# Optimization experiments

Measured on AMD Instinct MI355X. Metric: run time of the kernel, lower is better.

The kernel has to match this reference:

```python
import jax, jax.numpy as jnp
import numpy as np

# Module config (matches init_kwargs)
N_HEADS = 16
HEAD = 64
SEQ = 4096          # single prefill sequence (cu_seqlens_k = [0, SEQ])
BS = 64             # block_size (both q and k blocks)
LOCAL = 8           # local_blocks
VERT = 8            # vert_stride
NB = SEQ // BS      # number of blocks along seq
SLIDE = max(1, VERT // N_HEADS)  # get_head_sliding_step(16, 8, homo_head=False) -> 1
SM_SCALE = 1.0 / float(np.sqrt(HEAD))


def _build_layout():
    """Per-head block-sparse layout: causal + (local OR strided-vertical) blocks,
    padded to a fixed max nnz per row (CSR rows -> padded col indices + valid mask)."""
    h = np.arange(N_HEADS)[:, None, None]
    i = np.arange(NB)[None, :, None]
    j = np.arange(NB)[None, None, :]
    mask = (j <= i) & (((i - j) < LOCAL) | (((j + h * SLIDE + 1) % VERT) == 0))
    max_nnz = int(mask.sum(-1).max())
    cols = np.zeros((N_HEADS, NB, max_nnz), np.int32)
    valid = np.zeros((N_HEADS, NB, max_nnz), bool)
    for hh in range(N_HEADS):
        for ii in range(NB):
            c = np.nonzero(mask[hh, ii])[0]
            cols[hh, ii, :len(c)] = c
            valid[hh, ii, :len(c)] = True
    return cols, valid, max_nnz

_COLS_NP, _VALID_NP, MAX_NNZ = _build_layout()
COLS = jnp.asarray(_COLS_NP)    # [H, NB, NNZ] k-block ids (padded with 0)
VALID = jnp.asarray(_VALID_NP)  # [H, NB, NNZ] padding mask


def setup_inputs() -> dict:
    key = jax.random.key(0)
    kq, kk, kv = jax.random.split(key, 3)
    q = jax.random.normal(kq, (SEQ, N_HEADS, HEAD), jnp.float32)
    k = jax.random.normal(kk, (SEQ, N_HEADS, HEAD), jnp.float32)
    v = jax.random.normal(kv, (SEQ, N_HEADS, HEAD), jnp.float32)
    cu_seqlens_k = jnp.array([0, SEQ], jnp.int32)
    return {"q": q, "k": k, "v": v, "cu_seqlens_k": cu_seqlens_k}


def _attn(q, k, v):
    # [T, H, D] -> [H, NB, BS, D]
    qb = q.transpose(1, 0, 2).reshape(N_HEADS, NB, BS, HEAD)
    kb = k.transpose(1, 0, 2).reshape(N_HEADS, NB, BS, HEAD)
    vb = v.transpose(1, 0, 2).reshape(N_HEADS, NB, BS, HEAD)
    gather = jax.vmap(lambda x, c: x[c])  # per-head block gather
    kg = gather(kb, COLS)  # [H, NB, NNZ, BS, D]
    vg = gather(vb, COLS)  # [H, NB, NNZ, BS, D]
    # block-sparse scores: [H, NB(q blk), BS(m), NNZ(n), BS(j)]
    scores = jnp.einsum('himd,hinjd->himnj', qb, kg) * SM_SCALE
    qpos = jnp.arange(NB)[:, None] * BS + jnp.arange(BS)[None, :]   # [NB, BS]
    kpos = COLS[..., None] * BS + jnp.arange(BS)                    # [H, NB, NNZ, BS]
    allow = VALID[:, :, None, :, None] & (
        qpos[None, :, :, None, None] >= kpos[:, :, None, :, :])
    scores = jnp.where(allow, scores, -jnp.inf)
    p = jax.nn.softmax(scores.reshape(N_HEADS, NB, BS, MAX_NNZ * BS), axis=-1)
    p = p.reshape(N_HEADS, NB, BS, MAX_NNZ, BS)
    out = jnp.einsum('himnj,hinjd->himd', p, vg)
    return out.reshape(N_HEADS, SEQ, HEAD).transpose(1, 0, 2)  # [T, H, D]


def reference(q, k, v, cu_seqlens_k):
    # single-sequence prefill: past_len = 0, q_len == k_len == SEQ
    return _attn(q, k, v)
```

## Files before the change

kernel.cpp:

```cpp
#include <hip/hip_runtime.h>
#include <hip/hip_bf16.h>
#include <math.h>


#define NHEADS 16
#define HDIM   64
#define NBLK   64
#define SEQLEN 4096
#define KP     72
#define NEGBIG (-1.0e30f)

typedef __attribute__((ext_vector_type(8))) short bf16x8;
typedef __attribute__((ext_vector_type(4))) float f32x4;

__device__ __forceinline__ short f2bf(float x) {
    union { float f; unsigned u; } c; c.f = x;
    unsigned u = c.u;
    return (short)((u + 0x7FFFu + ((u >> 16) & 1u)) >> 16);
}
__device__ __forceinline__ short f2bf_trunc(float x) {
    union { float f; unsigned u; } c; c.f = x;
    return (short)(c.u >> 16);
}

__device__ __forceinline__ void load_lds16(const short* g, const short* l) {
    __builtin_amdgcn_global_load_lds(
        (const __attribute__((address_space(1))) void*)g,
        (__attribute__((address_space(3))) void*)l, 16, 0, 0);
}

__device__ __forceinline__ void drain_then_sync() {
    asm volatile("s_waitcnt vmcnt(0)" ::: "memory");
    __syncthreads();
}

__global__ __launch_bounds__(256)
void prep_kernel(const float* __restrict__ k, const float* __restrict__ v,
                 short* __restrict__ kt, short* __restrict__ vt) {
    __shared__ short tile[64 * KP];
    const int b = blockIdx.x;
    const int h = b >> 6, jb = b & 63;
    const int tid = threadIdx.x;

    #pragma unroll
    for (int it = 0; it < 4; ++it) {
        int e = it * 1024 + tid * 4;
        int key = e >> 6, d0 = e & 63;
        float4 f = *(const float4*)(v + ((size_t)(jb * 64 + key) * NHEADS + h) * HDIM + d0);
        tile[(d0 + 0) * KP + key] = f2bf(f.x);
        tile[(d0 + 1) * KP + key] = f2bf(f.y);
        tile[(d0 + 2) * KP + key] = f2bf(f.z);
        tile[(d0 + 3) * KP + key] = f2bf(f.w);
    }
    __syncthreads();
    short* vtile = vt + (size_t)b * 4096;
    #pragma unroll
    for (int ii = 0; ii < 2; ++ii) {
        int idx = ii * 256 + tid;
        int d = idx >> 3, gsw = idx & 7;
        int g = gsw ^ (d & 7);
        bf16x8 val;
        #pragma unroll
        for (int j = 0; j < 8; ++j) {
            int s   = g * 8 + j;
            int key = (s & 32) | (((s >> 2) & 1) << 4) | (((s >> 3) & 3) << 2) | (s & 3);
            val[j]  = tile[d * KP + key];
        }
        *(bf16x8*)(vtile + (size_t)idx * 8) = val;
    }
    short* ktile = kt + (size_t)b * 4096;
    #pragma unroll
    for (int ii = 0; ii < 2; ++ii) {
        int idx = ii * 256 + tid;
        int r = idx >> 3, g = idx & 7;
        const float* src = k + ((size_t)(jb * 64 + r) * NHEADS + h) * HDIM + g * 8;
        float4 f0 = *(const float4*)src;
        float4 f1 = *(const float4*)(src + 4);
        bf16x8 a;
        a[0]=f2bf(f0.x); a[1]=f2bf(f0.y); a[2]=f2bf(f0.z); a[3]=f2bf(f0.w);
        a[4]=f2bf(f1.x); a[5]=f2bf(f1.y); a[6]=f2bf(f1.z); a[7]=f2bf(f1.w);
        int G = r * 8 + (g ^ (r & 7));
        *(bf16x8*)(ktile + (size_t)G * 8) = a;
    }
}

__global__ __launch_bounds__(256, 4)
void attn_kernel(const short* __restrict__ kt, const short* __restrict__ vt,
                 const float* __restrict__ q, float* __restrict__ out) {
    __shared__ __align__(16) short kv[2 * 8192];

    const int b    = blockIdx.x;
    const int h    = ((b & 7) << 1) | ((b >> 3) & 1);
    const int idx  = b >> 4;
    const int qi   = (idx & 1) ? (63 - (idx >> 1)) : (idx >> 1);
    const int tid  = threadIdx.x;
    const int wave = tid >> 6;
    const int ih   = wave >> 1;
    const int jh   = wave & 1;
    const int lane = tid & 63;
    const int l16  = lane & 15;
    const int quad = lane >> 4;

    const int rowbase = qi * 64 + ih * 32;

    const float SC = 0.125f * 1.4426950408889634f;
    bf16x8 a_q[2][2];
    #pragma unroll
    for (int rg = 0; rg < 2; ++rg) {
        const float* qrow = q + ((size_t)(rowbase + rg * 16 + l16) * NHEADS + h) * HDIM;
        #pragma unroll
        for (int kk = 0; kk < 2; ++kk) {
            const float* src = qrow + kk * 32 + quad * 8;
            float4 f0 = *(const float4*)(src);
            float4 f1 = *(const float4*)(src + 4);
            bf16x8 a;
            a[0]=f2bf(f0.x*SC); a[1]=f2bf(f0.y*SC); a[2]=f2bf(f0.z*SC); a[3]=f2bf(f0.w*SC);
            a[4]=f2bf(f1.x*SC); a[5]=f2bf(f1.y*SC); a[6]=f2bf(f1.z*SC); a[7]=f2bf(f1.w*SC);
            a_q[rg][kk] = a;
        }
    }

    bf16x8 ones;
    #pragma unroll
    for (int j = 0; j < 8; ++j) ones[j] = (short)0x3F80;

    f32x4 o[2][4];
    f32x4 lacc[2];
    #pragma unroll
    for (int rg = 0; rg < 2; ++rg) {
        lacc[rg] = (f32x4){0.f,0.f,0.f,0.f};
        #pragma unroll
        for (int ntd = 0; ntd < 4; ++ntd) o[rg][ntd] = (f32x4){0.f,0.f,0.f,0.f};
    }

    const short* kth = kt + (size_t)(h * 64) * 4096;
    const short* vth = vt + (size_t)(h * 64) * 4096;

    const int j0  = (7 - h) & 7;
    const int l0  = (qi > 7) ? (qi - 7) : 0;
    const int nv  = (j0 < l0) ? ((l0 - j0 + 7) >> 3) : 0;
    const int T   = nv + (qi - l0 + 1);

    const int r7   = l16 & 7;
    const int gk0  = (quad ^ r7) * 8;
    const int gk1  = gk0 ^ 32;
    const int gv   = (((jh << 2) | quad) ^ r7) * 8;
    const int rowb = l16 * 64;
    const int krow0 = (jh * 32) * 64;

    {
        const int jb0 = (0 < nv) ? j0 : l0;
        const short* ktb = kth + (size_t)jb0 * 4096;
        const short* vtb = vth + (size_t)jb0 * 4096;
        load_lds16(ktb + (size_t)tid * 8,         &kv[wave * 512]);
        load_lds16(ktb + (size_t)(tid + 256) * 8, &kv[2048 + wave * 512]);
        load_lds16(vtb + (size_t)tid * 8,         &kv[4096 + wave * 512]);
        load_lds16(vtb + (size_t)(tid + 256) * 8, &kv[6144 + wave * 512]);
    }

    for (int t = 0; t < T; ++t) {
        drain_then_sync();

        if (t + 1 < T) {
            const int jn = (t + 1 < nv) ? (j0 + 8 * (t + 1)) : (l0 + (t + 1 - nv));
            const int bo = ((t + 1) & 1) * 8192;
            const short* ktb = kth + (size_t)jn * 4096;
            const short* vtb = vth + (size_t)jn * 4096;
            load_lds16(ktb + (size_t)tid * 8,         &kv[bo + wave * 512]);
            load_lds16(ktb + (size_t)(tid + 256) * 8, &kv[bo + 2048 + wave * 512]);
            load_lds16(vtb + (size_t)tid * 8,         &kv[bo + 4096 + wave * 512]);
            load_lds16(vtb + (size_t)(tid + 256) * 8, &kv[bo + 6144 + wave * 512]);
        }

        const short* kb = &kv[(t & 1) * 8192];
        const short* vb = kb + 4096;
        const bool diag = (t == T - 1);

        __builtin_amdgcn_s_setprio(1);

        bf16x8 kf0[2], kf1[2];
        #pragma unroll
        for (int kg = 0; kg < 2; ++kg) {
            kf0[kg] = *(const bf16x8*)&kb[krow0 + kg * 1024 + rowb + gk0];
            kf1[kg] = *(const bf16x8*)&kb[krow0 + kg * 1024 + rowb + gk1];
        }
        f32x4 s[2][2];
        #pragma unroll
        for (int kg = 0; kg < 2; ++kg) {
            #pragma unroll
            for (int rg = 0; rg < 2; ++rg) {
                f32x4 acc = (f32x4){0.f, 0.f, 0.f, 0.f};
                acc = __builtin_amdgcn_mfma_f32_16x16x32_bf16(kf0[kg], a_q[rg][0], acc, 0, 0, 0);
                acc = __builtin_amdgcn_mfma_f32_16x16x32_bf16(kf1[kg], a_q[rg][1], acc, 0, 0, 0);
                s[kg][rg] = acc;
            }
        }

        bf16x8 vf[4];
        #pragma unroll
        for (int ntd = 0; ntd < 4; ++ntd)
            vf[ntd] = *(const bf16x8*)&vb[ntd * 1024 + rowb + gv];

        short pb[2][2][4];
        #pragma unroll
        for (int kg = 0; kg < 2; ++kg) {
            #pragma unroll
            for (int rg = 0; rg < 2; ++rg) {
                #pragma unroll
                for (int r = 0; r < 4; ++r) {
                    const int keyl = jh * 32 + kg * 16 + quad * 4 + r;
                    const int qrl  = ih * 32 + rg * 16 + l16;
                    float raw = s[kg][rg][r];
                    raw = (diag && (keyl > qrl)) ? NEGBIG : raw;
                    float pv = __builtin_amdgcn_exp2f(raw);
                    pb[kg][rg][r] = f2bf_trunc(pv);
                }
            }
        }

        bf16x8 a_p[2];
        #pragma unroll
        for (int rg = 0; rg < 2; ++rg) {
            bf16x8 a;
            a[0]=pb[0][rg][0]; a[1]=pb[0][rg][1]; a[2]=pb[0][rg][2]; a[3]=pb[0][rg][3];
            a[4]=pb[1][rg][0]; a[5]=pb[1][rg][1]; a[6]=pb[1][rg][2]; a[7]=pb[1][rg][3];
            a_p[rg] = a;
        }

        #pragma unroll
        for (int rg = 0; rg < 2; ++rg) {
            #pragma unroll
            for (int ntd = 0; ntd < 4; ++ntd)
                o[rg][ntd] = __builtin_amdgcn_mfma_f32_16x16x32_bf16(a_p[rg], vf[ntd], o[rg][ntd], 0, 0, 0);
            lacc[rg] = __builtin_amdgcn_mfma_f32_16x16x32_bf16(a_p[rg], ones, lacc[rg], 0, 0, 0);
        }

        __builtin_amdgcn_s_setprio(0);
    }

    __syncthreads();
    f32x4* kvF = (f32x4*)kv;
    if (jh == 1) {
        #pragma unroll
        for (int rg = 0; rg < 2; ++rg) {
            #pragma unroll
            for (int ntd = 0; ntd < 4; ++ntd)
                kvF[(ih * 10 + rg * 4 + ntd) * 64 + lane] = o[rg][ntd];
            kvF[(ih * 10 + 8 + rg) * 64 + lane] = lacc[rg];
        }
    }
    __syncthreads();
    if (jh == 0) {
        #pragma unroll
        for (int rg = 0; rg < 2; ++rg) {
            #pragma unroll
            for (int ntd = 0; ntd < 4; ++ntd)
                o[rg][ntd] += kvF[(ih * 10 + rg * 4 + ntd) * 64 + lane];
            lacc[rg] += kvF[(ih * 10 + 8 + rg) * 64 + lane];
        }
        #pragma unroll
        for (int rg = 0; rg < 2; ++rg) {
            #pragma unroll
            for (int r = 0; r < 4; ++r) {
                const float invr = 1.0f / lacc[rg][r];
                int trow = rowbase + rg * 16 + quad * 4 + r;
                float* orow = out + ((size_t)trow * NHEADS + h) * HDIM;
                #pragma unroll
                for (int ntd = 0; ntd < 4; ++ntd)
                    orow[ntd * 16 + l16] = o[rg][ntd][r] * invr;
            }
        }
    }
}

extern "C" void kernel_launch(void* const* d_in, const int* in_sizes, int n_in,
                              void* d_out, int out_size, void* d_ws, size_t ws_size,
                              hipStream_t stream) {
    const float* q = (const float*)d_in[0];
    const float* k = (const float*)d_in[1];
    const float* v = (const float*)d_in[2];
    float* out = (float*)d_out;

    const size_t tileBytes = (size_t)NHEADS * NBLK * 4096 * sizeof(short);
    short* kt = (short*)d_ws;
    short* vt = (short*)((char*)d_ws + tileBytes);
    prep_kernel<<<dim3(NHEADS * NBLK), dim3(256), 0, stream>>>(k, v, kt, vt);
    attn_kernel<<<dim3(1024), dim3(256), 0, stream>>>(kt, vt, q, out);
}
```

Measured before the change: 111.7 us.

## Split attention block into two independent waves each owning half the keys

Reworks the attention kernel from 4 waves (2 query halves × 2 key halves) to 2 waves, where each wave covers all 64 query rows and loads its own half of each K/V block into private LDS double buffers. This removes the per-iteration block-wide barrier, leaving only a per-wave vmcnt wait, and halves the redundant K/V LDS reads across query halves. The V tile swizzle in the prep kernel is changed to match the new per-wave half-block layout, and the final reduction has each wave finish half of the rows. In exchange each wave holds twice the accumulators (more VGPRs), and with 128-thread blocks there are fewer waves per CU to hide latency.

```diff
diff --git a/kernel.cpp b/kernel.cpp
--- a/kernel.cpp
+++ b/kernel.cpp
@@ -27,11 +27,6 @@
     __builtin_amdgcn_global_load_lds(
         (const __attribute__((address_space(1))) void*)g,
         (__attribute__((address_space(3))) void*)l, 16, 0, 0);
-}
-
-__device__ __forceinline__ void drain_then_sync() {
-    asm volatile("s_waitcnt vmcnt(0)" ::: "memory");
-    __syncthreads();
 }
 
 __global__ __launch_bounds__(256)
@@ -57,8 +52,10 @@
     #pragma unroll
     for (int ii = 0; ii < 2; ++ii) {
         int idx = ii * 256 + tid;
-        int d = idx >> 3, gsw = idx & 7;
-        int g = gsw ^ (d & 7);
+        int jh = idx >> 8;
+        int d  = (idx >> 2) & 63;
+        int qq = idx & 3;
+        int g  = jh * 4 + (qq ^ ((d >> 1) & 3));
         bf16x8 val;
         #pragma unroll
         for (int j = 0; j < 8; ++j) {
@@ -84,30 +81,26 @@
     }
 }
 
-__global__ __launch_bounds__(256, 4)
+__global__ __launch_bounds__(128, 2)
 void attn_kernel(const short* __restrict__ kt, const short* __restrict__ vt,
                  const float* __restrict__ q, float* __restrict__ out) {
-    __shared__ __align__(16) short kv[2 * 8192];
+    __shared__ __align__(16) short kv[16384];
 
     const int b    = blockIdx.x;
     const int h    = ((b & 7) << 1) | ((b >> 3) & 1);
     const int idx  = b >> 4;
     const int qi   = (idx & 1) ? (63 - (idx >> 1)) : (idx >> 1);
     const int tid  = threadIdx.x;
-    const int wave = tid >> 6;
-    const int ih   = wave >> 1;
-    const int jh   = wave & 1;
+    const int jh   = tid >> 6;
     const int lane = tid & 63;
     const int l16  = lane & 15;
     const int quad = lane >> 4;
 
-    const int rowbase = qi * 64 + ih * 32;
-
     const float SC = 0.125f * 1.4426950408889634f;
-    bf16x8 a_q[2][2];
-    #pragma unroll
-    for (int rg = 0; rg < 2; ++rg) {
-        const float* qrow = q + ((size_t)(rowbase + rg * 16 + l16) * NHEADS + h) * HDIM;
+    bf16x8 a_q[4][2];
+    #pragma unroll
+    for (int rg = 0; rg < 4; ++rg) {
+        const float* qrow = q + ((size_t)(qi * 64 + rg * 16 + l16) * NHEADS + h) * HDIM;
         #pragma unroll
         for (int kk = 0; kk < 2; ++kk) {
             const float* src = qrow + kk * 32 + quad * 8;
@@ -124,10 +117,10 @@
     #pragma unroll
     for (int j = 0; j < 8; ++j) ones[j] = (short)0x3F80;
 
-    f32x4 o[2][4];
-    f32x4 lacc[2];
-    #pragma unroll
-    for (int rg = 0; rg < 2; ++rg) {
+    f32x4 o[4][4];
+    f32x4 lacc[4];
+    #pragma unroll
+    for (int rg = 0; rg < 4; ++rg) {
         lacc[rg] = (f32x4){0.f,0.f,0.f,0.f};
         #pragma unroll
         for (int ntd = 0; ntd < 4; ++ntd) o[rg][ntd] = (f32x4){0.f,0.f,0.f,0.f};
@@ -144,36 +137,39 @@
     const int r7   = l16 & 7;
     const int gk0  = (quad ^ r7) * 8;
     const int gk1  = gk0 ^ 32;
-    const int gv   = (((jh << 2) | quad) ^ r7) * 8;
     const int rowb = l16 * 64;
-    const int krow0 = (jh * 32) * 64;
+    const int vsw  = (l16 >> 1) & 3;
+    short* mylds = &kv[jh * 8192];
 
     {
         const int jb0 = (0 < nv) ? j0 : l0;
-        const short* ktb = kth + (size_t)jb0 * 4096;
-        const short* vtb = vth + (size_t)jb0 * 4096;
-        load_lds16(ktb + (size_t)tid * 8,         &kv[wave * 512]);
-        load_lds16(ktb + (size_t)(tid + 256) * 8, &kv[2048 + wave * 512]);
-        load_lds16(vtb + (size_t)tid * 8,         &kv[4096 + wave * 512]);
-        load_lds16(vtb + (size_t)(tid + 256) * 8, &kv[6144 + wave * 512]);
+        const short* ktb = kth + (size_t)jb0 * 4096 + jh * 2048;
+        const short* vtb = vth + (size_t)jb0 * 4096 + jh * 2048;
+        #pragma unroll
+        for (int ld = 0; ld < 4; ++ld) {
+            load_lds16(ktb + (size_t)(ld * 64 + lane) * 8, mylds + ld * 512);
+            load_lds16(vtb + (size_t)(ld * 64 + lane) * 8, mylds + 2048 + ld * 512);
+        }
     }
 
     for (int t = 0; t < T; ++t) {
-        drain_then_sync();
+        asm volatile("s_waitcnt vmcnt(0)" ::: "memory");
+        __builtin_amdgcn_sched_barrier(0);
 
         if (t + 1 < T) {
             const int jn = (t + 1 < nv) ? (j0 + 8 * (t + 1)) : (l0 + (t + 1 - nv));
-            const int bo = ((t + 1) & 1) * 8192;
-            const short* ktb = kth + (size_t)jn * 4096;
-            const short* vtb = vth + (size_t)jn * 4096;
-            load_lds16(ktb + (size_t)tid * 8,         &kv[bo + wave * 512]);
-            load_lds16(ktb + (size_t)(tid + 256) * 8, &kv[bo + 2048 + wave * 512]);
-            load_lds16(vtb + (size_t)tid * 8,         &kv[bo + 4096 + wave * 512]);
-            load_lds16(vtb + (size_t)(tid + 256) * 8, &kv[bo + 6144 + wave * 512]);
-        }
-
-        const short* kb = &kv[(t & 1) * 8192];
-        const short* vb = kb + 4096;
+            short* dst = mylds + ((t + 1) & 1) * 4096;
+            const short* ktb = kth + (size_t)jn * 4096 + jh * 2048;
+            const short* vtb = vth + (size_t)jn * 4096 + jh * 2048;
+            #pragma unroll
+            for (int ld = 0; ld < 4; ++ld) {
+                load_lds16(ktb + (size_t)(ld * 64 + lane) * 8, dst + ld * 512);
+                load_lds16(vtb + (size_t)(ld * 64 + lane) * 8, dst + 2048 + ld * 512);
+            }
+        }
+
+        const short* kb = mylds + (t & 1) * 4096;
+        const short* vb = kb + 2048;
         const bool diag = (t == T - 1);
 
         __builtin_amdgcn_s_setprio(1);
@@ -181,36 +177,27 @@
         bf16x8 kf0[2], kf1[2];
         #pragma unroll
         for (int kg = 0; kg < 2; ++kg) {
-            kf0[kg] = *(const bf16x8*)&kb[krow0 + kg * 1024 + rowb + gk0];
-            kf1[kg] = *(const bf16x8*)&kb[krow0 + kg * 1024 + rowb + gk1];
-        }
-        f32x4 s[2][2];
+            kf0[kg] = *(const bf16x8*)&kb[kg * 1024 + rowb + gk0];
+            kf1[kg] = *(const bf16x8*)&kb[kg * 1024 + rowb + gk1];
+        }
+        bf16x8 vf[4];
+        #pragma unroll
+        for (int ntd = 0; ntd < 4; ++ntd)
+            vf[ntd] = *(const bf16x8*)&vb[(ntd * 16 + l16) * 32 + (quad ^ vsw) * 8];
+
+        short pb[2][4][4];
         #pragma unroll
         for (int kg = 0; kg < 2; ++kg) {
             #pragma unroll
-            for (int rg = 0; rg < 2; ++rg) {
+            for (int rg = 0; rg < 4; ++rg) {
                 f32x4 acc = (f32x4){0.f, 0.f, 0.f, 0.f};
                 acc = __builtin_amdgcn_mfma_f32_16x16x32_bf16(kf0[kg], a_q[rg][0], acc, 0, 0, 0);
                 acc = __builtin_amdgcn_mfma_f32_16x16x32_bf16(kf1[kg], a_q[rg][1], acc, 0, 0, 0);
-                s[kg][rg] = acc;
-            }
-        }
-
-        bf16x8 vf[4];
-        #pragma unroll
-        for (int ntd = 0; ntd < 4; ++ntd)
-            vf[ntd] = *(const bf16x8*)&vb[ntd * 1024 + rowb + gv];
-
-        short pb[2][2][4];
-        #pragma unroll
-        for (int kg = 0; kg < 2; ++kg) {
-            #pragma unroll
-            for (int rg = 0; rg < 2; ++rg) {
                 #pragma unroll
                 for (int r = 0; r < 4; ++r) {
                     const int keyl = jh * 32 + kg * 16 + quad * 4 + r;
-                    const int qrl  = ih * 32 + rg * 16 + l16;
-                    float raw = s[kg][rg][r];
+                    const int qrl  = rg * 16 + l16;
+                    float raw = acc[r];
                     raw = (diag && (keyl > qrl)) ? NEGBIG : raw;
                     float pv = __builtin_amdgcn_exp2f(raw);
                     pb[kg][rg][r] = f2bf_trunc(pv);
@@ -218,57 +205,48 @@
             }
         }
 
-        bf16x8 a_p[2];
-        #pragma unroll
-        for (int rg = 0; rg < 2; ++rg) {
+        #pragma unroll
+        for (int rg = 0; rg < 4; ++rg) {
             bf16x8 a;
             a[0]=pb[0][rg][0]; a[1]=pb[0][rg][1]; a[2]=pb[0][rg][2]; a[3]=pb[0][rg][3];
             a[4]=pb[1][rg][0]; a[5]=pb[1][rg][1]; a[6]=pb[1][rg][2]; a[7]=pb[1][rg][3];
-            a_p[rg] = a;
-        }
-
-        #pragma unroll
-        for (int rg = 0; rg < 2; ++rg) {
             #pragma unroll
             for (int ntd = 0; ntd < 4; ++ntd)
-                o[rg][ntd] = __builtin_amdgcn_mfma_f32_16x16x32_bf16(a_p[rg], vf[ntd], o[rg][ntd], 0, 0, 0);
-            lacc[rg] = __builtin_amdgcn_mfma_f32_16x16x32_bf16(a_p[rg], ones, lacc[rg], 0, 0, 0);
+                o[rg][ntd] = __builtin_amdgcn_mfma_f32_16x16x32_bf16(a, vf[ntd], o[rg][ntd], 0, 0, 0);
+            lacc[rg] = __builtin_amdgcn_mfma_f32_16x16x32_bf16(a, ones, lacc[rg], 0, 0, 0);
         }
 
         __builtin_amdgcn_s_setprio(0);
     }
 
     __syncthreads();
-    f32x4* kvF = (f32x4*)kv;
-    if (jh == 1) {
-        #pragma unroll
-        for (int rg = 0; rg < 2; ++rg) {
+    f32x4* scr = (f32x4*)kv;
+    const int og0 = 2 * (1 - jh);
+    #pragma unroll
+    for (int rr = 0; rr < 2; ++rr) {
+        const int rg = og0 + rr;
+        #pragma unroll
+        for (int ntd = 0; ntd < 4; ++ntd)
+            scr[(rg * 5 + ntd) * 64 + lane] = o[rg][ntd];
+        scr[(rg * 5 + 4) * 64 + lane] = lacc[rg];
+    }
+    __syncthreads();
+    const int mg0 = 2 * jh;
+    #pragma unroll
+    for (int rr = 0; rr < 2; ++rr) {
+        const int rg = mg0 + rr;
+        #pragma unroll
+        for (int ntd = 0; ntd < 4; ++ntd)
+            o[rg][ntd] += scr[(rg * 5 + ntd) * 64 + lane];
+        lacc[rg] += scr[(rg * 5 + 4) * 64 + lane];
+        #pragma unroll
+        for (int r = 0; r < 4; ++r) {
+            const float invr = 1.0f / lacc[rg][r];
+            int trow = qi * 64 + rg * 16 + quad * 4 + r;
+            float* orow = out + ((size_t)trow * NHEADS + h) * HDIM;
             #pragma unroll
             for (int ntd = 0; ntd < 4; ++ntd)
-                kvF[(ih * 10 + rg * 4 + ntd) * 64 + lane] = o[rg][ntd];
-            kvF[(ih * 10 + 8 + rg) * 64 + lane] = lacc[rg];
-        }
-    }
-    __syncthreads();
-    if (jh == 0) {
-        #pragma unroll
-        for (int rg = 0; rg < 2; ++rg) {
-            #pragma unroll
-            for (int ntd = 0; ntd < 4; ++ntd)
-                o[rg][ntd] += kvF[(ih * 10 + rg * 4 + ntd) * 64 + lane];
-            lacc[rg] += kvF[(ih * 10 + 8 + rg) * 64 + lane];
-        }
-        #pragma unroll
-        for (int rg = 0; rg < 2; ++rg) {
-            #pragma unroll
-            for (int r = 0; r < 4; ++r) {
-                const float invr = 1.0f / lacc[rg][r];
-                int trow = rowbase + rg * 16 + quad * 4 + r;
-                float* orow = out + ((size_t)trow * NHEADS + h) * HDIM;
-                #pragma unroll
-                for (int ntd = 0; ntd < 4; ++ntd)
-                    orow[ntd * 16 + l16] = o[rg][ntd][r] * invr;
-            }
+                orow[ntd * 16 + l16] = o[rg][ntd][r] * invr;
         }
     }
 }
@@ -285,5 +263,5 @@
     short* kt = (short*)d_ws;
     short* vt = (short*)((char*)d_ws + tileBytes);
     prep_kernel<<<dim3(NHEADS * NBLK), dim3(256), 0, stream>>>(k, v, kt, vt);
-    attn_kernel<<<dim3(1024), dim3(256), 0, stream>>>(kt, vt, q, out);
-}
+    attn_kernel<<<dim3(1024), dim3(128), 0, stream>>>(kt, vt, q, out);
+}
```

After: 133.9 us. 19.8% more time.
